# Optimization experiments

Hardware: AMD Instinct MI355X
Metric: run time of the kernel (lower is better)

## Reference

```python
import jax, jax.numpy as jnp
import numpy as np

B, L, A, F = 4096, 12, 768, 4096  # batch, n_layers, d_activations, d_features


def setup_inputs() -> dict:
    key = jax.random.key(0)
    k_x, k_enc, k_dec, k_m, k_s = jax.random.split(key, 5)
    x = jax.random.normal(k_x, (B, L, A), dtype=jnp.float32)
    # Encoder: uniform(-1/sqrt(F), 1/sqrt(F)) per reset_parameters
    enc_thresh = 1.0 / np.sqrt(F)
    W_enc = jax.random.uniform(k_enc, (L, A, F), jnp.float32, -enc_thresh, enc_thresh)
    # Decoder: triangular weights W_i of shape (i+1, F, A), packed along axis 0.
    # Total rows = L*(L+1)//2. uniform(-1/sqrt(A*L), 1/sqrt(A*L)).
    dec_thresh = 1.0 / np.sqrt(A * L)
    n_tri = L * (L + 1) // 2
    W_dec_packed = jax.random.uniform(k_dec, (n_tri, F, A), jnp.float32, -dec_thresh, dec_thresh)
    # JumpReLU threshold per (layer, feature), init 0.03
    theta = jnp.full((L, F), 0.03, dtype=jnp.float32)
    # Dimensionwise input standardizer stats (per layer, per activation dim)
    in_mean = 0.1 * jax.random.normal(k_m, (L, A), dtype=jnp.float32)
    in_std = 1.0 + 0.1 * jax.random.uniform(k_s, (L, A), dtype=jnp.float32)
    return {"x": x, "in_mean": in_mean, "in_std": in_std, "W_enc": W_enc,
            "theta": theta, "W_dec_packed": W_dec_packed}


def reference(x, in_mean, in_std, W_enc, theta, W_dec_packed):
    # Input standardization: (x - mean) / std, broadcast over batch
    sx = (x - in_mean[None]) / in_std[None]                      # [B, L, A]
    # Encoder: per-layer dense projection
    enc = jnp.einsum('bla,laf->blf', sx, W_enc)                  # [B, L, F]
    # JumpReLU: x * (x > theta)
    act = enc * (enc > theta[None]).astype(enc.dtype)            # [B, L, F]
    # Decoder: triangular accumulation. Layer i reads features of layers 0..i
    # with its own weight tensor W_i (slice of the packed triangular buffer).
    n_layers = W_enc.shape[0]
    preds = []
    off = 0
    for i in range(n_layers):
        W_i = W_dec_packed[off:off + i + 1]                      # [i+1, F, A]
        preds.append(jnp.einsum('blf,lfa->ba', act[:, :i + 1], W_i))
        off += i + 1
    logits = jnp.stack(preds, axis=1)                            # [B, L, A]
    # Original forward returns (logits, encoder_out, concat_w_dec); the
    # concat_w_dec list is just a reshape of the decoder params, omitted here.
    return logits, enc
```

## Files before the change

kernel.cpp:

```cpp
#include <hip/hip_runtime.h>
#include <cstdint>
#include <cstddef>

#define B_ 4096
#define L_ 12
#define A_ 768
#define F_ 4096
#define NTRI 78

typedef __bf16 bf16x8 __attribute__((ext_vector_type(8)));
typedef float f32x4 __attribute__((ext_vector_type(4)));
typedef unsigned short u16x4 __attribute__((ext_vector_type(4)));

__device__ __forceinline__ unsigned short f32_to_bf16(float f) {
  unsigned int u = __float_as_uint(f);
  u += 0x7fffu + ((u >> 16) & 1u);
  return (unsigned short)(u >> 16);
}

__device__ __forceinline__ void gload_lds16(const void* g, void* l) {
  __builtin_amdgcn_global_load_lds(
      (const __attribute__((address_space(1))) void*)g,
      (__attribute__((address_space(3))) void*)l,
      16, 0, 0);
}

__global__ __launch_bounds__(256) void prep_sx(
    const float* __restrict__ x, const float* __restrict__ mean,
    const float* __restrict__ stdv, unsigned short* __restrict__ sx) {
  size_t i4 = (size_t)blockIdx.x * 256 + threadIdx.x;
  size_t e = i4 * 4;
  if (e >= (size_t)B_ * L_ * A_) return;
  unsigned int a = (unsigned int)(e % A_);
  unsigned int t = (unsigned int)(e / A_);
  unsigned int b = t / L_;
  unsigned int l = t % L_;
  float4 xv = *(const float4*)(x + e);
  float4 mv = *(const float4*)(mean + (size_t)l * A_ + a);
  float4 sv = *(const float4*)(stdv + (size_t)l * A_ + a);
  u16x4 o;
  o.x = f32_to_bf16((xv.x - mv.x) / sv.x);
  o.y = f32_to_bf16((xv.y - mv.y) / sv.y);
  o.z = f32_to_bf16((xv.z - mv.z) / sv.z);
  o.w = f32_to_bf16((xv.w - mv.w) / sv.w);
  *(u16x4*)(sx + ((size_t)l * B_ + b) * A_ + a) = o;
}

__global__ __launch_bounds__(256) void transpose_cvt(
    const float* __restrict__ in, unsigned short* __restrict__ out,
    int R, int C) {
  __shared__ float tile[32][33];
  const float* inz = in + (size_t)blockIdx.z * R * C;
  unsigned short* outz = out + (size_t)blockIdx.z * R * C;
  int c0 = blockIdx.x * 32, r0 = blockIdx.y * 32;
  int tx = threadIdx.x, ty = threadIdx.y;
#pragma unroll
  for (int q = 0; q < 4; ++q) {
    int r = ty + q * 8;
    tile[r][tx] = inz[(size_t)(r0 + r) * C + (c0 + tx)];
  }
  __syncthreads();
#pragma unroll
  for (int q = 0; q < 4; ++q) {
    int r = ty + q * 8;
    outz[(size_t)(c0 + r) * R + (r0 + tx)] = f32_to_bf16(tile[tx][r]);
  }
}

__device__ __forceinline__ bf16x8 read_frag(const char* base, int row, int g) {
  int ss = g ^ ((row >> 1) & 3);
  return *(const bf16x8*)(base + row * 64 + ss * 16);
}

template <class FSrc>
__device__ __forceinline__ void stage_tile(FSrc src, int kt, char* ringbase,
                                           int w, int lane) {
  char* base = ringbase + (kt & 3) * 16384;
#pragma unroll
  for (int q = 0; q < 2; ++q) {
    int c = q * 8 + w;
    int row = c * 16 + (lane >> 2);
    int ss = (lane & 3) ^ ((row >> 1) & 3);
    gload_lds16(src(kt, row, ss * 8), base + c * 1024);
  }
}

template <class FA, class FB>
__device__ __forceinline__ void gemm_core(int KT, char* AS, char* BS, int w,
                                          int lane, int wr, int wc, FA srcA,
                                          FB srcB, f32x4 (&acc)[8][4]) {
  const int g = lane >> 4;
  const int fr = lane & 15;
  stage_tile(srcA, 0, AS, w, lane);
  stage_tile(srcB, 0, BS, w, lane);
  stage_tile(srcA, 1, AS, w, lane);
  stage_tile(srcB, 1, BS, w, lane);
  stage_tile(srcA, 2, AS, w, lane);
  stage_tile(srcB, 2, BS, w, lane);
  asm volatile("s_waitcnt vmcnt(8)" ::: "memory");
  __builtin_amdgcn_s_barrier();

  for (int kt = 0; kt < KT; ++kt) {
    const char* Ab = AS + (kt & 3) * 16384;
    const char* Bb = BS + (kt & 3) * 16384;
    bf16x8 bfr[4], afr[4];
#pragma unroll
    for (int ni = 0; ni < 4; ++ni)
      bfr[ni] = read_frag(Bb, wc * 64 + ni * 16 + fr, g);
#pragma unroll
    for (int mi = 0; mi < 4; ++mi)
      afr[mi] = read_frag(Ab, wr * 128 + mi * 16 + fr, g);
    if (kt + 3 < KT) stage_tile(srcA, kt + 3, AS, w, lane);
    asm volatile("" ::: "memory");
    __builtin_amdgcn_s_barrier();
    __builtin_amdgcn_s_setprio(1);
#pragma unroll
    for (int mi = 0; mi < 4; ++mi)
#pragma unroll
      for (int ni = 0; ni < 4; ++ni)
        acc[mi][ni] = __builtin_amdgcn_mfma_f32_16x16x32_bf16(
            afr[mi], bfr[ni], acc[mi][ni], 0, 0, 0);
    __builtin_amdgcn_s_setprio(0);
    asm volatile("" ::: "memory");
    __builtin_amdgcn_s_barrier();
#pragma unroll
    for (int mi = 0; mi < 4; ++mi)
      afr[mi] = read_frag(Ab, wr * 128 + (mi + 4) * 16 + fr, g);
    if (kt + 3 < KT) stage_tile(srcB, kt + 3, BS, w, lane);
    asm volatile("" ::: "memory");
    __builtin_amdgcn_s_barrier();
    __builtin_amdgcn_s_setprio(1);
#pragma unroll
    for (int mi = 0; mi < 4; ++mi)
#pragma unroll
      for (int ni = 0; ni < 4; ++ni)
        acc[mi + 4][ni] = __builtin_amdgcn_mfma_f32_16x16x32_bf16(
            afr[mi], bfr[ni], acc[mi + 4][ni], 0, 0, 0);
    __builtin_amdgcn_s_setprio(0);
    if (kt + 3 < KT)      { asm volatile("s_waitcnt vmcnt(8)" ::: "memory"); }
    else if (kt + 2 < KT) { asm volatile("s_waitcnt vmcnt(4)" ::: "memory"); }
    else if (kt + 1 < KT) { asm volatile("s_waitcnt vmcnt(0)" ::: "memory"); }
    asm volatile("" ::: "memory");
    __builtin_amdgcn_s_barrier();
  }
}

__global__ __launch_bounds__(512, 2) void enc_gemm8(
    const unsigned short* __restrict__ sxT,
    const unsigned short* __restrict__ wT,
    const float* __restrict__ theta,
    float* __restrict__ enc_out,
    unsigned short* __restrict__ act)
{
  extern __shared__ __align__(16) char lds[];
  char* AS = lds;
  char* BS = lds + 65536;
  const int b = blockIdx.x;
  const int wg = (b & 7) * 384 + (b >> 3);
  const int l = wg >> 8;
  const int blk = wg & 255;
  const int m0 = (blk & 15) * 256;
  const int n0 = (blk >> 4) * 256;
  const int tid = threadIdx.x;
  const int w = tid >> 6, lane = tid & 63;
  const int wr = w >> 2, wc = w & 3;

  f32x4 acc[8][4] = {};
  auto srcA = [&](int kt, int row, int ce) {
    return sxT + ((size_t)l * B_ + m0 + row) * A_ + kt * 32 + ce;
  };
  auto srcB = [&](int kt, int row, int ce) {
    return wT + ((size_t)l * F_ + n0 + row) * A_ + kt * 32 + ce;
  };
  gemm_core(A_ / 32, AS, BS, w, lane, wr, wc, srcA, srcB, acc);

  const int g = lane >> 4, fr = lane & 15;
#pragma unroll
  for (int ni = 0; ni < 4; ++ni) {
    const int gcol = n0 + wc * 64 + ni * 16 + fr;
    const float th = theta[(size_t)l * F_ + gcol];
#pragma unroll
    for (int mi = 0; mi < 8; ++mi) {
      const int growb = m0 + wr * 128 + mi * 16 + g * 4;
#pragma unroll
      for (int jj = 0; jj < 4; ++jj) {
        const float v = acc[mi][ni][jj];
        const size_t grow = (size_t)(growb + jj);
        enc_out[(grow * L_ + l) * F_ + gcol] = v;
        act[((size_t)l * B_ + grow) * F_ + gcol] =
            (v > th) ? f32_to_bf16(v) : (unsigned short)0;
      }
    }
  }
}

__global__ __launch_bounds__(512, 2) void dec_gemm8(
    const unsigned short* __restrict__ act,
    const unsigned short* __restrict__ wdecT,
    float* __restrict__ logits)
{
  extern __shared__ __align__(16) char lds[];
  char* AS = lds;
  char* BS = lds + 65536;
  const int b = blockIdx.x;
  const int xcd = b & 7;
  const int idx = b >> 3;
  const int z = idx / 6;
  const int j = idx - z * 6;
  const int i = 11 - z;
  const int blk = xcd * 6 + j;
  const int m0 = (blk & 15) * 256;
  const int n0 = (blk >> 4) * 256;
  const int triBase = i * (i + 1) / 2;
  const int KT = (i + 1) * 128;
  const int tid = threadIdx.x;
  const int w = tid >> 6, lane = tid & 63;
  const int wr = w >> 2, wc = w & 3;

  f32x4 acc[8][4] = {};
  auto srcA = [&](int kt, int row, int ce) {
    int l = kt >> 7;
    int kk0 = (kt & 127) * 32;
    return act + ((size_t)l * B_ + m0 + row) * F_ + kk0 + ce;
  };
  auto srcB = [&](int kt, int row, int ce) {
    int l = kt >> 7;
    int kk0 = (kt & 127) * 32;
    return wdecT + ((size_t)(triBase + l) * A_ + n0 + row) * F_ + kk0 + ce;
  };
  gemm_core(KT, AS, BS, w, lane, wr, wc, srcA, srcB, acc);

  const int g = lane >> 4, fr = lane & 15;
#pragma unroll
  for (int mi = 0; mi < 8; ++mi) {
    const int growb = m0 + wr * 128 + mi * 16 + g * 4;
#pragma unroll
    for (int ni = 0; ni < 4; ++ni) {
      const int gcol = n0 + wc * 64 + ni * 16 + fr;
#pragma unroll
      for (int jj = 0; jj < 4; ++jj)
        logits[((size_t)(growb + jj) * L_ + i) * A_ + gcol] = acc[mi][ni][jj];
    }
  }
}

extern "C" void kernel_launch(void* const* d_in, const int* in_sizes, int n_in,
                              void* d_out, int out_size, void* d_ws,
                              size_t ws_size, hipStream_t stream) {
  (void)in_sizes; (void)n_in; (void)out_size; (void)ws_size;
  const float* x = (const float*)d_in[0];
  const float* mean = (const float*)d_in[1];
  const float* stdv = (const float*)d_in[2];
  const float* Wenc = (const float*)d_in[3];
  const float* theta = (const float*)d_in[4];
  const float* Wdec = (const float*)d_in[5];

  float* logits = (float*)d_out;
  float* enc = (float*)d_out + (size_t)B_ * L_ * A_;

  char* ws = (char*)d_ws;
  const size_t actBytes = (size_t)L_ * B_ * F_ * 2;
  const size_t sxBytes = (size_t)L_ * B_ * A_ * 2;
  unsigned short* act = (unsigned short*)ws;
  unsigned short* sx = (unsigned short*)(ws + actBytes);
  unsigned short* wencT = (unsigned short*)(ws + actBytes + sxBytes);
  unsigned short* wdecT = (unsigned short*)(ws + actBytes);

  hipFuncSetAttribute((const void*)enc_gemm8,
                      hipFuncAttributeMaxDynamicSharedMemorySize, 131072);
  hipFuncSetAttribute((const void*)dec_gemm8,
                      hipFuncAttributeMaxDynamicSharedMemorySize, 131072);

  prep_sx<<<(B_ * L_ * A_ / 4 + 255) / 256, 256, 0, stream>>>(x, mean, stdv, sx);
  transpose_cvt<<<dim3(F_ / 32, A_ / 32, L_), dim3(32, 8), 0, stream>>>(
      Wenc, wencT, A_, F_);
  enc_gemm8<<<3072, 512, 131072, stream>>>(sx, wencT, theta, enc, act);
  transpose_cvt<<<dim3(A_ / 32, F_ / 32, NTRI), dim3(32, 8), 0, stream>>>(
      Wdec, wdecT, F_, A_);
  dec_gemm8<<<576, 512, 131072, stream>>>(act, wdecT, logits);
}
```

Before: 3.001 ms.

## Software-pipeline LDS fragment reads in GEMM core and widen weight transpose tiles

The GEMM main loop now prefetches the next k-tile's B and first-half A fragments from LDS while the current MFMAs run. It issues both global-to-LDS stages together and cuts the per-iteration barriers from four to one. Separately, the weight transpose-and-convert kernel uses 64x64 tiles with float4 loads and 16-byte bf16 stores in place of 32x32 scalar accesses. The pipelining holds more fragment registers live, which may hurt occupancy, and the single barrier changes how ring-buffer slot reuse is synchronised.

```diff
diff --git a/kernel.cpp b/kernel.cpp
--- a/kernel.cpp
+++ b/kernel.cpp
@@ -11,6 +11,7 @@
 typedef __bf16 bf16x8 __attribute__((ext_vector_type(8)));
 typedef float f32x4 __attribute__((ext_vector_type(4)));
 typedef unsigned short u16x4 __attribute__((ext_vector_type(4)));
+typedef unsigned short u16x8 __attribute__((ext_vector_type(8)));
 
 __device__ __forceinline__ unsigned short f32_to_bf16(float f) {
   unsigned int u = __float_as_uint(f);
@@ -46,24 +47,36 @@
   *(u16x4*)(sx + ((size_t)l * B_ + b) * A_ + a) = o;
 }
 
-__global__ __launch_bounds__(256) void transpose_cvt(
+__global__ __launch_bounds__(256) void transpose_cvt64(
     const float* __restrict__ in, unsigned short* __restrict__ out,
     int R, int C) {
-  __shared__ float tile[32][33];
+  __shared__ float tile[64][65];
   const float* inz = in + (size_t)blockIdx.z * R * C;
   unsigned short* outz = out + (size_t)blockIdx.z * R * C;
-  int c0 = blockIdx.x * 32, r0 = blockIdx.y * 32;
-  int tx = threadIdx.x, ty = threadIdx.y;
-#pragma unroll
-  for (int q = 0; q < 4; ++q) {
-    int r = ty + q * 8;
-    tile[r][tx] = inz[(size_t)(r0 + r) * C + (c0 + tx)];
+  const int c0 = blockIdx.x * 64, r0 = blockIdx.y * 64;
+  const int t = threadIdx.x;
+  {
+    const int c = (t & 15) * 4;
+    const int rb = t >> 4;
+#pragma unroll
+    for (int q = 0; q < 4; ++q) {
+      const int r = rb + q * 16;
+      float4 v = *(const float4*)(inz + (size_t)(r0 + r) * C + (c0 + c));
+      tile[r][c] = v.x; tile[r][c + 1] = v.y;
+      tile[r][c + 2] = v.z; tile[r][c + 3] = v.w;
+    }
   }
   __syncthreads();
-#pragma unroll
-  for (int q = 0; q < 4; ++q) {
-    int r = ty + q * 8;
-    outz[(size_t)(c0 + r) * R + (r0 + tx)] = f32_to_bf16(tile[tx][r]);
+  {
+    const int c = t >> 2;
+    const int rb = (t & 3) * 16;
+#pragma unroll
+    for (int h = 0; h < 2; ++h) {
+      u16x8 o;
+#pragma unroll
+      for (int j = 0; j < 8; ++j) o[j] = f32_to_bf16(tile[rb + h * 8 + j][c]);
+      *(u16x8*)(outz + (size_t)(c0 + c) * R + (r0 + rb + h * 8)) = o;
+    }
   }
 }
 
@@ -100,48 +113,58 @@
   asm volatile("s_waitcnt vmcnt(8)" ::: "memory");
   __builtin_amdgcn_s_barrier();
 
+  bf16x8 bcur[4], a0cur[4], a1[4], bnxt[4], a0nxt[4];
+#pragma unroll
+  for (int ni = 0; ni < 4; ++ni)
+    bcur[ni] = read_frag(BS, wc * 64 + ni * 16 + fr, g);
+#pragma unroll
+  for (int mi = 0; mi < 4; ++mi)
+    a0cur[mi] = read_frag(AS, wr * 128 + mi * 16 + fr, g);
+
   for (int kt = 0; kt < KT; ++kt) {
     const char* Ab = AS + (kt & 3) * 16384;
     const char* Bb = BS + (kt & 3) * 16384;
-    bf16x8 bfr[4], afr[4];
-#pragma unroll
-    for (int ni = 0; ni < 4; ++ni)
-      bfr[ni] = read_frag(Bb, wc * 64 + ni * 16 + fr, g);
+    const char* Abn = AS + ((kt + 1) & 3) * 16384;
+    const char* Bbn = BS + ((kt + 1) & 3) * 16384;
+    if (kt + 2 < KT) { asm volatile("s_waitcnt vmcnt(4)" ::: "memory"); }
+    else             { asm volatile("s_waitcnt vmcnt(0)" ::: "memory"); }
+    __builtin_amdgcn_s_barrier();
 #pragma unroll
     for (int mi = 0; mi < 4; ++mi)
-      afr[mi] = read_frag(Ab, wr * 128 + mi * 16 + fr, g);
-    if (kt + 3 < KT) stage_tile(srcA, kt + 3, AS, w, lane);
-    asm volatile("" ::: "memory");
-    __builtin_amdgcn_s_barrier();
+      a1[mi] = read_frag(Ab, wr * 128 + (mi + 4) * 16 + fr, g);
+    if (kt + 3 < KT) {
+      stage_tile(srcA, kt + 3, AS, w, lane);
+      stage_tile(srcB, kt + 3, BS, w, lane);
+    }
     __builtin_amdgcn_s_setprio(1);
 #pragma unroll
     for (int mi = 0; mi < 4; ++mi)
 #pragma unroll
       for (int ni = 0; ni < 4; ++ni)
         acc[mi][ni] = __builtin_amdgcn_mfma_f32_16x16x32_bf16(
-            afr[mi], bfr[ni], acc[mi][ni], 0, 0, 0);
+            a0cur[mi], bcur[ni], acc[mi][ni], 0, 0, 0);
     __builtin_amdgcn_s_setprio(0);
-    asm volatile("" ::: "memory");
-    __builtin_amdgcn_s_barrier();
-#pragma unroll
-    for (int mi = 0; mi < 4; ++mi)
-      afr[mi] = read_frag(Ab, wr * 128 + (mi + 4) * 16 + fr, g);
-    if (kt + 3 < KT) stage_tile(srcB, kt + 3, BS, w, lane);
-    asm volatile("" ::: "memory");
-    __builtin_amdgcn_s_barrier();
+    if (kt + 1 < KT) {
+#pragma unroll
+      for (int ni = 0; ni < 4; ++ni)
+        bnxt[ni] = read_frag(Bbn, wc * 64 + ni * 16 + fr, g);
+#pragma unroll
+      for (int mi = 0; mi < 4; ++mi)
+        a0nxt[mi] = read_frag(Abn, wr * 128 + mi * 16 + fr, g);
+    }
     __builtin_amdgcn_s_setprio(1);
 #pragma unroll
     for (int mi = 0; mi < 4; ++mi)
 #pragma unroll
       for (int ni = 0; ni < 4; ++ni)
         acc[mi + 4][ni] = __builtin_amdgcn_mfma_f32_16x16x32_bf16(
-            afr[mi], bfr[ni], acc[mi + 4][ni], 0, 0, 0);
+            a1[mi], bcur[ni], acc[mi + 4][ni], 0, 0, 0);
     __builtin_amdgcn_s_setprio(0);
-    if (kt + 3 < KT)      { asm volatile("s_waitcnt vmcnt(8)" ::: "memory"); }
-    else if (kt + 2 < KT) { asm volatile("s_waitcnt vmcnt(4)" ::: "memory"); }
-    else if (kt + 1 < KT) { asm volatile("s_waitcnt vmcnt(0)" ::: "memory"); }
-    asm volatile("" ::: "memory");
-    __builtin_amdgcn_s_barrier();
+#pragma unroll
+    for (int q = 0; q < 4; ++q) {
+      bcur[q] = bnxt[q];
+      a0cur[q] = a0nxt[q];
+    }
   }
 }
 
@@ -272,10 +295,10 @@
                       hipFuncAttributeMaxDynamicSharedMemorySize, 131072);
 
   prep_sx<<<(B_ * L_ * A_ / 4 + 255) / 256, 256, 0, stream>>>(x, mean, stdv, sx);
-  transpose_cvt<<<dim3(F_ / 32, A_ / 32, L_), dim3(32, 8), 0, stream>>>(
+  transpose_cvt64<<<dim3(F_ / 64, A_ / 64, L_), 256, 0, stream>>>(
       Wenc, wencT, A_, F_);
   enc_gemm8<<<3072, 512, 131072, stream>>>(sx, wencT, theta, enc, act);
-  transpose_cvt<<<dim3(A_ / 32, F_ / 32, NTRI), dim3(32, 8), 0, stream>>>(
+  transpose_cvt64<<<dim3(A_ / 64, F_ / 64, NTRI), 256, 0, stream>>>(
       Wdec, wdecT, F_, A_);
   dec_gemm8<<<576, 512, 131072, stream>>>(act, wdecT, logits);
 }
```

Result: no change. 2.960 ms (-1.4%).
